# Optimization experiments

Measured on AMD Instinct MI355X. Metric: run time of the kernel, lower is better.

## Reference

```python
import jax, jax.numpy as jnp
import numpy as np

EPS = 1e-9


def _scatter_mean(msg, idx, num_segments):
    # msg: [E, D], idx: [E] -> [num_segments, D] mean of messages per segment
    s = jax.ops.segment_sum(msg, idx, num_segments=num_segments)
    c = jax.ops.segment_sum(jnp.ones((idx.shape[0], 1), msg.dtype), idx, num_segments=num_segments)
    return s / (c + EPS)


def _knn_smooth(x, k=5):
    # Euclidean cdist + (k+1) nearest neighbors (incl. self), mean of neighbor embeddings
    sq = jnp.sum(x * x, axis=1)  # [U]
    d2 = sq[:, None] + sq[None, :] - 2.0 * (x @ x.T)  # [U, U]
    dist = jnp.sqrt(jnp.maximum(d2, 0.0))
    _, idx = jax.lax.top_k(-dist, k + 1)  # smallest distances
    return x[idx].mean(axis=1)  # [U, D]


def setup_inputs() -> dict:
    key = jax.random.key(0)
    ks = jax.random.split(key, 16)
    U, P, T, W, S, DW, MW, E, D = 10000, 50000, 48, 10, 4, 400, 12, 1000000, 128
    return {
        "user_emb": jax.random.normal(ks[0], (U, D), jnp.float32),
        "poi_emb": jax.random.normal(ks[1], (P, D), jnp.float32),
        "time_emb": jax.random.normal(ks[2], (T, D), jnp.float32),
        "weather_emb": jax.random.normal(ks[3], (W, D), jnp.float32),
        "season_emb": jax.random.normal(ks[4], (S, D), jnp.float32),
        "day_weather_emb": jax.random.normal(ks[5], (DW, D), jnp.float32),
        "month_weather_emb": jax.random.normal(ks[6], (MW, D), jnp.float32),
        "e_W_per_edge": jax.random.normal(ks[7], (E, D), jnp.float32),
        "u_idx": jax.random.randint(ks[8], (E,), 0, U, jnp.int32),
        "p_idx": jax.random.randint(ks[9], (E,), 0, P, jnp.int32),
        "t_idx": jax.random.randint(ks[10], (E,), 0, T, jnp.int32),
        "s_idx": jax.random.randint(ks[11], (E,), 0, S, jnp.int32),
        "w_now_idx": jax.random.randint(ks[12], (E,), 0, W, jnp.int32),
        "w_day_idx": jax.random.randint(ks[13], (E, 3), 0, DW, jnp.int32),
        "w_month_idx": jax.random.randint(ks[14], (E,), 0, MW, jnp.int32),
    }


def reference(user_emb, poi_emb, time_emb, weather_emb, season_emb, day_weather_emb,
              month_weather_emb, e_W_per_edge, u_idx, p_idx, t_idx, s_idx,
              w_now_idx, w_day_idx, w_month_idx):
    u_gath = user_emb[u_idx]          # [E, D]
    p_gath = poi_emb[p_idx]           # [E, D]
    t_gath = time_emb[t_idx]          # [E, D]

    new_user = _scatter_mean(p_gath + t_gath + e_W_per_edge, u_idx, user_emb.shape[0])
    new_poi = _scatter_mean(u_gath + t_gath + e_W_per_edge, p_idx, poi_emb.shape[0])

    msg_up = u_gath + p_gath          # shared message user+poi
    new_time = _scatter_mean(msg_up, t_idx, time_emb.shape[0])
    new_season = _scatter_mean(msg_up, s_idx, season_emb.shape[0])
    new_weather = _scatter_mean(msg_up, w_now_idx, weather_emb.shape[0])

    new_user = _knn_smooth(new_user, k=5)

    # day-weather: each edge contributes to yesterday/today/tomorrow nodes
    msg_day = jnp.repeat(msg_up, 3, axis=0)        # [3E, D]
    day_idx = w_day_idx.reshape(-1)                # [3E]
    new_day = _scatter_mean(msg_day, day_idx, day_weather_emb.shape[0])

    new_month = _scatter_mean(msg_up, w_month_idx, month_weather_emb.shape[0])

    return (new_user, new_poi, new_time, new_weather, new_season, new_day, new_month)
```

## Files before the change

### kernel.cpp

```cpp
#include <hip/hip_runtime.h>
#include <math.h>

#define U_N 10000
#define P_N 50000
#define T_N 48
#define W_N 10
#define S_N 4
#define DW_N 400
#define MW_N 12
#define E_N 1000000
#define XR 10112
#define NCH 8
#define CT 79
#define EPSF 1e-9f
#define NCOL 474
#define CSTR 480

#define OFF_CNT_U   0
#define OFF_CNT_P   10000
#define OFF_OFF_U   60000
#define OFF_OFF_P   70016
#define OFF_CUR_U   120032
#define OFF_CUR_P   130032
#define OFF_UPACK   180032
#define OFF_PPACK   4180032
#define OFF_CU      8180032
#define OFF_CP      9380032
#define OFF_ACC474  15380032
#define OFF_CNTALL  15441472
#define OFF_X       15441952
#define OFF_SQ      16736288

#define O_USER 0
#define O_POI  1280000
#define O_TIME 7680000
#define O_WEA  7686144
#define O_SEA  7687424
#define O_DAY  7687936
#define O_MON  7739136

__global__ __launch_bounds__(256) void k_hist(
    const int* __restrict__ u_idx, const int* __restrict__ p_idx,
    int* __restrict__ cnt_u, int* __restrict__ cnt_p)
{
    for (int e = blockIdx.x * 256 + threadIdx.x; e < E_N; e += gridDim.x * 256) {
        atomicAdd(&cnt_u[u_idx[e]], 1);
        atomicAdd(&cnt_p[p_idx[e]], 1);
    }
}

__global__ __launch_bounds__(1024) void k_scan(
    const int* __restrict__ cnt_u, int* __restrict__ off_u, int* __restrict__ cur_u,
    const int* __restrict__ cnt_p, int* __restrict__ off_p, int* __restrict__ cur_p)
{
    const int n = (blockIdx.x == 0) ? U_N : P_N;
    const int* cnt = (blockIdx.x == 0) ? cnt_u : cnt_p;
    int* off = (blockIdx.x == 0) ? off_u : off_p;
    int* cur = (blockIdx.x == 0) ? cur_u : cur_p;
    __shared__ int sd[1024];
    int per = (n + 1023) >> 10;
    int base = threadIdx.x * per;
    int s = 0;
    for (int j = 0; j < per; j++) {
        int idx = base + j;
        if (idx < n) s += cnt[idx];
    }
    sd[threadIdx.x] = s;
    __syncthreads();
    for (int d = 1; d < 1024; d <<= 1) {
        int t = (threadIdx.x >= d) ? sd[threadIdx.x - d] : 0;
        __syncthreads();
        sd[threadIdx.x] += t;
        __syncthreads();
    }
    int run = sd[threadIdx.x] - s;
    for (int j = 0; j < per; j++) {
        int idx = base + j;
        if (idx < n) {
            off[idx] = run;
            cur[idx] = run;
            run += cnt[idx];
        }
    }
    if (threadIdx.x == 1023) off[n] = sd[1023];
}

__global__ __launch_bounds__(256) void k_scatter(
    const int* __restrict__ u_idx, const int* __restrict__ p_idx,
    const int* __restrict__ t_idx, const int* __restrict__ s_idx,
    const int* __restrict__ wn_idx, const int* __restrict__ wd_idx,
    const int* __restrict__ wm_idx,
    int* __restrict__ cur_u, int* __restrict__ cur_p,
    int4* __restrict__ upack, int4* __restrict__ ppack)
{
    for (int e = blockIdx.x * 256 + threadIdx.x; e < E_N; e += gridDim.x * 256) {
        int u = u_idx[e], p = p_idx[e], t = t_idx[e];
        int s = s_idx[e], wn = wn_idx[e], wm = wm_idx[e];
        int d0 = wd_idx[e * 3 + 0], d1 = wd_idx[e * 3 + 1], d2 = wd_idx[e * 3 + 2];
        int w0 = e | (t << 20);
        int sp = (s << 16) | (wn << 18) | (wm << 22);
        int dp = d0 | (d1 << 9) | (d2 << 18);
        int pu = atomicAdd(&cur_u[u], 1);
        upack[pu] = make_int4(w0, p | sp, dp, 0);
        int pp = atomicAdd(&cur_p[p], 1);
        ppack[pp] = make_int4(w0, u | sp, dp, 0);
    }
}

__global__ __launch_bounds__(256) void k_seg(
    const int4* __restrict__ pack, const int* __restrict__ off,
    const float2* __restrict__ oemb, const float2* __restrict__ temb,
    const float2* __restrict__ ew, unsigned char* __restrict__ Cmat,
    float2* __restrict__ outv, float* __restrict__ sq,
    int nseg, int nreal, int mode)
{
    __shared__ int hist[4][CSTR];
    int wv = threadIdx.x >> 6;
    int lane = threadIdx.x & 63;
    int seg = blockIdx.x * 4 + wv;
    if (seg >= nseg) return;

    if (seg >= nreal) {
        outv[(size_t)seg * 64 + lane] = make_float2(0.f, 0.f);
        if (mode == 1 && lane == 0) sq[seg] = INFINITY;
        return;
    }

    int* h = hist[wv];
    for (int i = lane; i < CSTR; i += 64) h[i] = 0;

    int o0 = off[seg], o1 = off[seg + 1];
    float2 acc = make_float2(0.f, 0.f);

    int4 pk = make_int4(0, 0, 0, 0);
    if (o0 < o1) pk = pack[o0];
    for (int i = o0; i < o1; ++i) {
        int4 nx = pk;
        if (i + 1 < o1) nx = pack[i + 1];
        int e = pk.x & 0xFFFFF, t = (pk.x >> 20) & 63;
        int oth = pk.y & 0xFFFF;
        int s = (pk.y >> 16) & 3, wn = (pk.y >> 18) & 15, wm = (pk.y >> 22) & 15;
        int q0 = pk.z & 511, q1 = (pk.z >> 9) & 511, q2 = (pk.z >> 18) & 511;

        float2 wf = ew[(size_t)e * 64 + lane];
        float2 ov = oemb[(size_t)oth * 64 + lane];
        float2 tv = temb[t * 64 + lane];
        acc.x += ov.x + tv.x + wf.x;
        acc.y += ov.y + tv.y + wf.y;

        int b = t;
        b = (lane == 1) ? 48 + s : b;
        b = (lane == 2) ? 52 + wn : b;
        b = (lane == 3) ? 62 + wm : b;
        b = (lane == 4) ? 74 + q0 : b;
        b = (lane == 5) ? 74 + q1 : b;
        b = (lane == 6) ? 74 + q2 : b;
        if (lane < 7) atomicAdd(&h[b], 1);
        pk = nx;
    }

    float den = (float)(o1 - o0) + EPSF;
    float2 xm = make_float2(acc.x / den, acc.y / den);
    outv[(size_t)seg * 64 + lane] = xm;

    if (mode == 1) {
        float d = xm.x * xm.x + xm.y * xm.y;
        for (int m = 32; m >= 1; m >>= 1) d += __shfl_xor(d, m);
        if (lane == 0) sq[seg] = d;
    }

    unsigned char* crow = Cmat + (size_t)seg * CSTR;
    for (int i = lane; i < CSTR / 4; i += 64) {
        uchar4 v;
        v.x = (unsigned char)h[4 * i + 0];
        v.y = (unsigned char)h[4 * i + 1];
        v.z = (unsigned char)h[4 * i + 2];
        v.w = (unsigned char)h[4 * i + 3];
        *(uchar4*)&crow[4 * i] = v;
    }
}

#define DTILE 32
#define KB 16

__global__ __launch_bounds__(256) void k_cgemm(
    const float* __restrict__ emb, const unsigned char* __restrict__ C,
    int K, int kper, float* __restrict__ acc474, float* __restrict__ cnt_all,
    int do_cnt)
{
    __shared__ __align__(16) float se[KB][128];
    __shared__ __align__(16) float scf[KB][DTILE];
    int d0 = blockIdx.x * DTILE;
    int k0 = blockIdx.y * kper;
    int k1 = min(K, k0 + kper);
    int n2 = (threadIdx.x & 63) * 2;
    int dg = threadIdx.x >> 6;
    int dbase = dg * 8;
    bool cntth = do_cnt && ((threadIdx.x & 63) == 0);

    float acc[8][2];
    float ca[8];
#pragma unroll
    for (int j = 0; j < 8; j++) { acc[j][0] = 0.f; acc[j][1] = 0.f; ca[j] = 0.f; }

    for (int kb = k0; kb < k1; kb += KB) {
        __syncthreads();
        for (int t = threadIdx.x; t < KB * 64; t += 256) {
            int kk = t >> 6, cc = (t & 63) * 2;
            float2 v = make_float2(0.f, 0.f);
            if (kb + kk < k1) v = *(const float2*)&emb[(size_t)(kb + kk) * 128 + cc];
            *(float2*)&se[kk][cc] = v;
        }
        for (int t = threadIdx.x; t < KB * DTILE; t += 256) {
            int kk = t >> 5, dd = t & 31;
            scf[kk][dd] = (kb + kk < k1 && d0 + dd < NCOL)
                          ? (float)C[(size_t)(kb + kk) * CSTR + d0 + dd] : 0.f;
        }
        __syncthreads();
#pragma unroll 4
        for (int kk = 0; kk < KB; kk++) {
            float2 e = *(const float2*)&se[kk][n2];
            float4 c0 = *(const float4*)&scf[kk][dbase];
            float4 c1 = *(const float4*)&scf[kk][dbase + 4];
            float cf[8] = { c0.x, c0.y, c0.z, c0.w, c1.x, c1.y, c1.z, c1.w };
#pragma unroll
            for (int j = 0; j < 8; j++) {
                acc[j][0] = fmaf(cf[j], e.x, acc[j][0]);
                acc[j][1] = fmaf(cf[j], e.y, acc[j][1]);
            }
            if (cntth) {
#pragma unroll
                for (int j = 0; j < 8; j++) ca[j] += cf[j];
            }
        }
    }
#pragma unroll
    for (int j = 0; j < 8; j++) {
        int d = d0 + dbase + j;
        if (d < NCOL) {
            unsafeAtomicAdd(&acc474[d * 128 + n2], acc[j][0]);
            unsafeAtomicAdd(&acc474[d * 128 + n2 + 1], acc[j][1]);
        }
    }
    if (cntth) {
#pragma unroll
        for (int j = 0; j < 8; j++) {
            int d = d0 + dbase + j;
            if (d < NCOL) unsafeAtomicAdd(&cnt_all[d], ca[j]);
        }
    }
}

__global__ __launch_bounds__(256) void k_norm_all(
    const float* __restrict__ acc474, const float* __restrict__ cnt_all,
    float* __restrict__ out)
{
    int idx = blockIdx.x * 256 + threadIdx.x;
    int row = idx >> 7, c = idx & 127;
    float v = acc474[idx] / (cnt_all[row] + EPSF);
    int off;
    if (row < 48)      off = O_TIME + row * 128 + c;
    else if (row < 52) off = O_SEA + (row - 48) * 128 + c;
    else if (row < 62) off = O_WEA + (row - 52) * 128 + c;
    else if (row < 74) off = O_MON + (row - 62) * 128 + c;
    else               off = O_DAY + (row - 74) * 128 + c;
    out[off] = v;
}

#define KNN_PAD 134

__device__ inline void ins6(unsigned long long (&l)[6], unsigned long long cand) {
    if (cand < l[5]) {
        l[5] = cand;
#pragma unroll
        for (int k = 5; k >= 1; k--) {
            unsigned long long a = l[k - 1], b = l[k];
            l[k - 1] = (b < a) ? b : a;
            l[k] = (b < a) ? a : b;
        }
    }
}

__global__ __launch_bounds__(256) void k_knn(
    const float* __restrict__ X, const float* __restrict__ sq,
    unsigned long long* __restrict__ lists)
{
    __shared__ __align__(16) unsigned char smem[49152];
    float* Ab = (float*)smem;
    float* Bb = Ab + 32 * KNN_PAD;
    unsigned long long* mb = (unsigned long long*)smem;

    int rb = blockIdx.x / NCH, ch = blockIdx.x % NCH;
    int row0 = rb * 128;
    int tid = threadIdx.x;
    int tr = tid >> 3;
    int tc = tid & 7;

    float sqr[4];
#pragma unroll
    for (int i = 0; i < 4; i++) sqr[i] = sq[row0 + tr * 4 + i];

    unsigned long long lst[4][6];
#pragma unroll
    for (int i = 0; i < 4; i++)
#pragma unroll
        for (int k = 0; k < 6; k++) lst[i][k] = ~0ull;

    for (int ct = ch; ct < CT; ct += NCH) {
        int col0 = ct * 128;
        float acc[4][16];
#pragma unroll
        for (int i = 0; i < 4; i++)
#pragma unroll
            for (int j = 0; j < 16; j++) acc[i][j] = 0.f;

        for (int kc = 0; kc < 4; kc++) {
            __syncthreads();
#pragma unroll
            for (int i = 0; i < 16; i++) {
                int lin = i * 256 + tid;
                int r = lin >> 5, kk = lin & 31;
                Ab[kk * KNN_PAD + r] = X[(row0 + r) * 128 + kc * 32 + kk];
                Bb[kk * KNN_PAD + r] = X[(col0 + r) * 128 + kc * 32 + kk];
            }
            __syncthreads();
#pragma unroll 2
            for (int kk = 0; kk < 32; kk++) {
                float a[4], b[16];
                float2 t0 = *(const float2*)&Ab[kk * KNN_PAD + tr * 4];
                float2 t1 = *(const float2*)&Ab[kk * KNN_PAD + tr * 4 + 2];
                a[0] = t0.x; a[1] = t0.y; a[2] = t1.x; a[3] = t1.y;
#pragma unroll
                for (int j = 0; j < 8; j++) {
                    float2 tb = *(const float2*)&Bb[kk * KNN_PAD + tc * 16 + j * 2];
                    b[2 * j] = tb.x; b[2 * j + 1] = tb.y;
                }
#pragma unroll
                for (int i = 0; i < 4; i++)
#pragma unroll
                    for (int j = 0; j < 16; j++)
                        acc[i][j] = fmaf(a[i], b[j], acc[i][j]);
            }
        }
#pragma unroll
        for (int j = 0; j < 16; j++) {
            int col = col0 + tc * 16 + j;
            float sqc = sq[col];
#pragma unroll
            for (int i = 0; i < 4; i++) {
                float d2 = fmaxf(fmaf(-2.f, acc[i][j], sqr[i] + sqc), 0.f);
                unsigned long long cand =
                    ((unsigned long long)__float_as_uint(d2) << 32) | (unsigned)col;
                ins6(lst[i], cand);
            }
        }
    }
    __syncthreads();
#pragma unroll
    for (int i = 0; i < 4; i++)
#pragma unroll
        for (int k = 0; k < 6; k++)
            mb[((tr * 4 + i) * 8 + tc) * 6 + k] = lst[i][k];
    __syncthreads();
    if (tid < 128) {
        unsigned long long outl[6];
#pragma unroll
        for (int k = 0; k < 6; k++) outl[k] = ~0ull;
        for (int t = 0; t < 8; t++)
            for (int k = 0; k < 6; k++)
                ins6(outl, mb[(tid * 8 + t) * 6 + k]);
#pragma unroll
        for (int k = 0; k < 6; k++)
            lists[((size_t)(row0 + tid) * NCH + ch) * 6 + k] = outl[k];
    }
}

__global__ __launch_bounds__(256) void k_final(
    const unsigned long long* __restrict__ lists,
    const float* __restrict__ X, float* __restrict__ out)
{
    int row = blockIdx.x * 4 + (threadIdx.x >> 6);
    int ln = threadIdx.x & 63;
    unsigned long long l[6];
#pragma unroll
    for (int k = 0; k < 6; k++) l[k] = ~0ull;
    if (ln == 0) {
        for (int t = 0; t < NCH; t++)
            for (int k = 0; k < 6; k++)
                ins6(l, lists[((size_t)row * NCH + t) * 6 + k]);
    }
    float s0 = 0.f, s1 = 0.f;
#pragma unroll
    for (int k = 0; k < 6; k++) {
        int idx = __shfl((int)(unsigned)l[k], 0);
        s0 += X[idx * 128 + ln];
        s1 += X[idx * 128 + 64 + ln];
    }
    out[row * 128 + ln] = s0 * (1.f / 6.f);
    out[row * 128 + 64 + ln] = s1 * (1.f / 6.f);
}

extern "C" void kernel_launch(void* const* d_in, const int* in_sizes, int n_in,
                              void* d_out, int out_size, void* d_ws, size_t ws_size,
                              hipStream_t stream) {
    const float* uemb = (const float*)d_in[0];
    const float* pemb = (const float*)d_in[1];
    const float2* temb2 = (const float2*)d_in[2];
    const float2* ew2 = (const float2*)d_in[7];
    const int* u_idx = (const int*)d_in[8];
    const int* p_idx = (const int*)d_in[9];
    const int* t_idx = (const int*)d_in[10];
    const int* s_idx = (const int*)d_in[11];
    const int* wn_idx = (const int*)d_in[12];
    const int* wd_idx = (const int*)d_in[13];
    const int* wm_idx = (const int*)d_in[14];

    float* out = (float*)d_out;
    float* ws = (float*)d_ws;

    int* cnt_u = (int*)(ws + OFF_CNT_U);
    int* cnt_p = (int*)(ws + OFF_CNT_P);
    int* off_u = (int*)(ws + OFF_OFF_U);
    int* off_p = (int*)(ws + OFF_OFF_P);
    int* cur_u = (int*)(ws + OFF_CUR_U);
    int* cur_p = (int*)(ws + OFF_CUR_P);
    int4* upack = (int4*)(ws + OFF_UPACK);
    int4* ppack = (int4*)(ws + OFF_PPACK);
    unsigned char* Cu = (unsigned char*)(ws + OFF_CU);
    unsigned char* Cp = (unsigned char*)(ws + OFF_CP);
    float* acc474 = ws + OFF_ACC474;
    float* cnt_all = ws + OFF_CNTALL;
    float* X = ws + OFF_X;
    float* sqv = ws + OFF_SQ;
    unsigned long long* lists = (unsigned long long*)(ws + OFF_UPACK);

    hipMemsetAsync(ws, 0, 60000 * sizeof(float), stream);
    hipMemsetAsync(ws + OFF_ACC474, 0, (61440 + 480) * sizeof(float), stream);

    k_hist<<<512, 256, 0, stream>>>(u_idx, p_idx, cnt_u, cnt_p);
    k_scan<<<2, 1024, 0, stream>>>(cnt_u, off_u, cur_u, cnt_p, off_p, cur_p);
    k_scatter<<<1024, 256, 0, stream>>>(u_idx, p_idx, t_idx, s_idx, wn_idx, wd_idx,
                                        wm_idx, cur_u, cur_p, upack, ppack);

    k_seg<<<12500, 256, 0, stream>>>(ppack, off_p, (const float2*)uemb, temb2, ew2,
                                     Cp, (float2*)(out + O_POI), nullptr,
                                     P_N, P_N, 0);
    k_seg<<<2528, 256, 0, stream>>>(upack, off_u, (const float2*)pemb, temb2, ew2,
                                    Cu, (float2*)X, sqv,
                                    XR, U_N, 1);

    k_cgemm<<<dim3(15, 8), 256, 0, stream>>>(uemb, Cu, U_N, 1250, acc474, cnt_all, 1);
    k_cgemm<<<dim3(15, 40), 256, 0, stream>>>(pemb, Cp, P_N, 1250, acc474, cnt_all, 0);
    k_norm_all<<<237, 256, 0, stream>>>(acc474, cnt_all, out);

    k_knn<<<CT * NCH, 256, 0, stream>>>(X, sqv, lists);
    k_final<<<U_N / 4, 256, 0, stream>>>(lists, X, out + O_USER);
}
```

Baseline: 2.852 ms.

## Widen cgemm D-tile, double KNN chunks, merge KNN lists via wave shuffles

Doubles the cgemm column tile so each thread accumulates 16 output rows, halving the grid along D and reloading the embedding tile half as often. Splits the KNN column sweep into 16 chunks instead of 8 for more blocks and parallelism. Interleaves B columns across threads, and replaces the shared-memory top-6 merge with xor-shuffle merges across the 8 lanes that share a row. The costs are more registers in cgemm, and more partial lists for k_final to merge.

```diff
diff --git a/kernel.cpp b/kernel.cpp
--- a/kernel.cpp
+++ b/kernel.cpp
@@ -10,7 +10,7 @@
 #define MW_N 12
 #define E_N 1000000
 #define XR 10112
-#define NCH 8
+#define NCH 16
 #define CT 79
 #define EPSF 1e-9f
 #define NCOL 474
@@ -180,7 +180,7 @@
     }
 }
 
-#define DTILE 32
+#define DTILE 64
 #define KB 16
 
 __global__ __launch_bounds__(256) void k_cgemm(
@@ -195,13 +195,13 @@
     int k1 = min(K, k0 + kper);
     int n2 = (threadIdx.x & 63) * 2;
     int dg = threadIdx.x >> 6;
-    int dbase = dg * 8;
+    int dbase = dg * 16;
     bool cntth = do_cnt && ((threadIdx.x & 63) == 0);
 
-    float acc[8][2];
-    float ca[8];
-#pragma unroll
-    for (int j = 0; j < 8; j++) { acc[j][0] = 0.f; acc[j][1] = 0.f; ca[j] = 0.f; }
+    float acc[16][2];
+    float ca[16];
+#pragma unroll
+    for (int j = 0; j < 16; j++) { acc[j][0] = 0.f; acc[j][1] = 0.f; ca[j] = 0.f; }
 
     for (int kb = k0; kb < k1; kb += KB) {
         __syncthreads();
@@ -212,7 +212,7 @@
             *(float2*)&se[kk][cc] = v;
         }
         for (int t = threadIdx.x; t < KB * DTILE; t += 256) {
-            int kk = t >> 5, dd = t & 31;
+            int kk = t >> 6, dd = t & 63;
             scf[kk][dd] = (kb + kk < k1 && d0 + dd < NCOL)
                           ? (float)C[(size_t)(kb + kk) * CSTR + d0 + dd] : 0.f;
         }
@@ -220,22 +220,26 @@
 #pragma unroll 4
         for (int kk = 0; kk < KB; kk++) {
             float2 e = *(const float2*)&se[kk][n2];
-            float4 c0 = *(const float4*)&scf[kk][dbase];
-            float4 c1 = *(const float4*)&scf[kk][dbase + 4];
-            float cf[8] = { c0.x, c0.y, c0.z, c0.w, c1.x, c1.y, c1.z, c1.w };
-#pragma unroll
-            for (int j = 0; j < 8; j++) {
+            float cf[16];
+#pragma unroll
+            for (int q = 0; q < 4; q++) {
+                float4 c = *(const float4*)&scf[kk][dbase + q * 4];
+                cf[q * 4 + 0] = c.x; cf[q * 4 + 1] = c.y;
+                cf[q * 4 + 2] = c.z; cf[q * 4 + 3] = c.w;
+            }
+#pragma unroll
+            for (int j = 0; j < 16; j++) {
                 acc[j][0] = fmaf(cf[j], e.x, acc[j][0]);
                 acc[j][1] = fmaf(cf[j], e.y, acc[j][1]);
             }
             if (cntth) {
 #pragma unroll
-                for (int j = 0; j < 8; j++) ca[j] += cf[j];
-            }
-        }
-    }
-#pragma unroll
-    for (int j = 0; j < 8; j++) {
+                for (int j = 0; j < 16; j++) ca[j] += cf[j];
+            }
+        }
+    }
+#pragma unroll
+    for (int j = 0; j < 16; j++) {
         int d = d0 + dbase + j;
         if (d < NCOL) {
             unsafeAtomicAdd(&acc474[d * 128 + n2], acc[j][0]);
@@ -244,7 +248,7 @@
     }
     if (cntth) {
 #pragma unroll
-        for (int j = 0; j < 8; j++) {
+        for (int j = 0; j < 16; j++) {
             int d = d0 + dbase + j;
             if (d < NCOL) unsafeAtomicAdd(&cnt_all[d], ca[j]);
         }
@@ -285,10 +289,8 @@
     const float* __restrict__ X, const float* __restrict__ sq,
     unsigned long long* __restrict__ lists)
 {
-    __shared__ __align__(16) unsigned char smem[49152];
-    float* Ab = (float*)smem;
-    float* Bb = Ab + 32 * KNN_PAD;
-    unsigned long long* mb = (unsigned long long*)smem;
+    __shared__ __align__(16) float Ab[32 * KNN_PAD];
+    __shared__ __align__(16) float Bb[32 * KNN_PAD];
 
     int rb = blockIdx.x / NCH, ch = blockIdx.x % NCH;
     int row0 = rb * 128;
@@ -332,7 +334,7 @@
                 a[0] = t0.x; a[1] = t0.y; a[2] = t1.x; a[3] = t1.y;
 #pragma unroll
                 for (int j = 0; j < 8; j++) {
-                    float2 tb = *(const float2*)&Bb[kk * KNN_PAD + tc * 16 + j * 2];
+                    float2 tb = *(const float2*)&Bb[kk * KNN_PAD + tc * 2 + j * 16];
                     b[2 * j] = tb.x; b[2 * j + 1] = tb.y;
                 }
 #pragma unroll
@@ -343,35 +345,42 @@
             }
         }
 #pragma unroll
-        for (int j = 0; j < 16; j++) {
-            int col = col0 + tc * 16 + j;
-            float sqc = sq[col];
+        for (int j = 0; j < 8; j++) {
+            int c0 = col0 + tc * 2 + j * 16;
+            float sq0 = sq[c0], sq1 = sq[c0 + 1];
 #pragma unroll
             for (int i = 0; i < 4; i++) {
-                float d2 = fmaxf(fmaf(-2.f, acc[i][j], sqr[i] + sqc), 0.f);
-                unsigned long long cand =
-                    ((unsigned long long)__float_as_uint(d2) << 32) | (unsigned)col;
-                ins6(lst[i], cand);
-            }
-        }
-    }
-    __syncthreads();
-#pragma unroll
-    for (int i = 0; i < 4; i++)
-#pragma unroll
-        for (int k = 0; k < 6; k++)
-            mb[((tr * 4 + i) * 8 + tc) * 6 + k] = lst[i][k];
-    __syncthreads();
-    if (tid < 128) {
-        unsigned long long outl[6];
-#pragma unroll
-        for (int k = 0; k < 6; k++) outl[k] = ~0ull;
-        for (int t = 0; t < 8; t++)
+                float d20 = fmaxf(fmaf(-2.f, acc[i][2 * j], sqr[i] + sq0), 0.f);
+                float d21 = fmaxf(fmaf(-2.f, acc[i][2 * j + 1], sqr[i] + sq1), 0.f);
+                ins6(lst[i], ((unsigned long long)__float_as_uint(d20) << 32) | (unsigned)c0);
+                ins6(lst[i], ((unsigned long long)__float_as_uint(d21) << 32) | (unsigned)(c0 + 1));
+            }
+        }
+    }
+
+#pragma unroll
+    for (int m = 1; m <= 4; m <<= 1) {
+#pragma unroll
+        for (int i = 0; i < 4; i++) {
+            unsigned long long tmp[6];
+#pragma unroll
+            for (int k = 0; k < 6; k++) tmp[k] = lst[i][k];
+#pragma unroll
+            for (int k = 0; k < 6; k++) {
+                unsigned lo = (unsigned)(tmp[k] & 0xffffffffull);
+                unsigned hi = (unsigned)(tmp[k] >> 32);
+                lo = (unsigned)__shfl_xor((int)lo, m);
+                hi = (unsigned)__shfl_xor((int)hi, m);
+                ins6(lst[i], ((unsigned long long)hi << 32) | lo);
+            }
+        }
+    }
+    if (tc == 0) {
+#pragma unroll
+        for (int i = 0; i < 4; i++)
+#pragma unroll
             for (int k = 0; k < 6; k++)
-                ins6(outl, mb[(tid * 8 + t) * 6 + k]);
-#pragma unroll
-        for (int k = 0; k < 6; k++)
-            lists[((size_t)(row0 + tid) * NCH + ch) * 6 + k] = outl[k];
+                lists[((size_t)(row0 + tr * 4 + i) * NCH + ch) * 6 + k] = lst[i][k];
     }
 }
 
@@ -449,8 +458,8 @@
                                     Cu, (float2*)X, sqv,
                                     XR, U_N, 1);
 
-    k_cgemm<<<dim3(15, 8), 256, 0, stream>>>(uemb, Cu, U_N, 1250, acc474, cnt_all, 1);
-    k_cgemm<<<dim3(15, 40), 256, 0, stream>>>(pemb, Cp, P_N, 1250, acc474, cnt_all, 0);
+    k_cgemm<<<dim3(8, 8), 256, 0, stream>>>(uemb, Cu, U_N, 1250, acc474, cnt_all, 1);
+    k_cgemm<<<dim3(8, 40), 256, 0, stream>>>(pemb, Cp, P_N, 1250, acc474, cnt_all, 0);
     k_norm_all<<<237, 256, 0, stream>>>(acc474, cnt_all, out);
 
     k_knn<<<CT * NCH, 256, 0, stream>>>(X, sqv, lists);
```

Measured after the change: 2.687 ms. 1.06x faster.
